# Performance work log

Measured on AMD Instinct MI355X. Metric: run time of the kernel, lower is better.

Reference implementation:

```python
import jax, jax.numpy as jnp
from jax import lax
import numpy as np

IMG = 800
SUB = 16
FS = IMG // SUB            # 50
NA = 9                     # 3 ratios x 3 scales
PRE_NMS = 6000             # test-mode n_test_pre_nms
POST_NMS = 300             # test-mode n_test_post_nms
NMS_THRESH = 0.7
MIN_BOX = 16.0
SLOPE = 0.01               # nn.LeakyReLU default


def build_anchors():
    # Faithful to _generate_anchor: x outer loop, y inner; ctr = grid - 8;
    # anchor rows are [x1, y1, w, h]; ratio outer, scale inner.
    c = np.arange(SUB, (FS + 1) * SUB, SUB).astype(np.float32) - 8.0  # 50 centers
    cx = np.repeat(c, FS)   # x is the outer loop
    cy = np.tile(c, FS)     # y is the inner loop
    rs = np.array([0.5, 1.0, 2.0], dtype=np.float32)
    ss = np.array([8.0, 16.0, 32.0], dtype=np.float32)
    hs = (SUB * ss[None, :] * np.sqrt(rs)[:, None]).reshape(-1)        # [9]
    ws = (SUB * ss[None, :] * np.sqrt(1.0 / rs)[:, None]).reshape(-1)  # [9]
    x1 = cx[:, None] - ws[None, :] / 2.0   # [2500, 9]
    y1 = cy[:, None] - hs[None, :] / 2.0
    w = np.broadcast_to(ws[None, :], x1.shape)
    h = np.broadcast_to(hs[None, :], x1.shape)
    return np.stack([x1, y1, w, h], axis=-1).reshape(-1, 4).astype(np.float32)  # [22500, 4]


def _conv(x, w, b, pad):
    y = lax.conv_general_dilated(x, w, (1, 1), ((pad, pad), (pad, pad)),
                                 dimension_numbers=("NCHW", "OIHW", "NCHW"))
    return y + b[None, :, None, None]


def _nms_keep(boxes):
    # Greedy NMS over score-sorted boxes [P,4] = (x1,y1,x2,y2); returns keep mask.
    x1, y1, x2, y2 = boxes[:, 0], boxes[:, 1], boxes[:, 2], boxes[:, 3]
    area = (x2 - x1 + 1.0) * (y2 - y1 + 1.0)
    P = boxes.shape[0]
    idx = jnp.arange(P)

    def body(i, keep):
        xx1 = jnp.maximum(x1[i], x1)
        yy1 = jnp.maximum(y1[i], y1)
        xx2 = jnp.minimum(x2[i], x2)
        yy2 = jnp.maximum(y2[i], y2)  # faithful to source bug: np.maximum, not minimum
        w = jnp.maximum(0.0, xx2 - xx1 + 1.0)
        h = jnp.maximum(0.0, yy2 - yy1 + 1.0)
        inter = w * h
        ov = inter / (area[i] + area - inter)
        suppress = (ov > NMS_THRESH) & (idx > i) & keep[i]
        return keep & ~suppress

    return lax.fori_loop(0, P, body, jnp.ones((P,), dtype=bool))


def _forward(in_features, conv_w, conv_b, reg_w, reg_b, cls_w, cls_b):
    B = in_features.shape[0]
    feat = _conv(in_features, conv_w, conv_b, 1)
    feat = jnp.where(feat >= 0, feat, SLOPE * feat)  # LeakyReLU(0.01)
    reg = _conv(feat, reg_w, reg_b, 0).transpose(0, 2, 3, 1).reshape(B, -1, 4)
    cls = _conv(feat, cls_w, cls_b, 0).transpose(0, 2, 3, 1).reshape(B, -1, 2)
    cls = jax.nn.softmax(cls, axis=2)

    anchors = jnp.asarray(build_anchors())  # [A,4] = (x1,y1,w,h)
    # The torch loop overwrites `rois` each batch iteration and returns only the
    # last batch's proposals; compute that directly.
    pr = reg[-1]                 # [A,4]
    score = cls[-1, :, 1]        # [A]
    hi = jnp.float32(IMG - 1)
    rx1 = jnp.clip(pr[:, 0] + anchors[:, 0], 0.0, hi)
    ry1 = jnp.clip(pr[:, 1] + anchors[:, 1], 0.0, hi)
    rx2 = jnp.clip(pr[:, 0] + anchors[:, 0] + pr[:, 2] + anchors[:, 2], 0.0, hi)
    ry2 = jnp.clip(pr[:, 1] + anchors[:, 1] + pr[:, 3] + anchors[:, 3], 0.0, hi)
    w = pr[:, 2] + anchors[:, 2]  # unclipped, as in source
    h = pr[:, 3] + anchors[:, 3]
    valid = (w >= MIN_BOX) & (h >= MIN_BOX)
    s = jnp.where(valid, score, -jnp.inf)   # filtered boxes sort to the end
    order = jnp.argsort(-s)[:PRE_NMS]       # top-6000 valid by objectness
    boxes = jnp.stack([rx1, ry1, rx2, ry2], axis=1)[order]  # [PRE,4]

    keep = _nms_keep(lax.stop_gradient(boxes))
    # first POST_NMS surviving boxes, in score order
    sel = jnp.argsort(jnp.where(keep, jnp.arange(PRE_NMS), PRE_NMS))[:POST_NMS]
    kb = boxes[sel]
    # output format: x1, y1, w, h
    return jnp.stack([kb[:, 0], kb[:, 1],
                      kb[:, 2] - kb[:, 0] + 1.0,
                      kb[:, 3] - kb[:, 1] + 1.0], axis=1)


def setup_inputs() -> dict:
    key = jax.random.key(0)
    k = jax.random.split(key, 4)
    return {
        "in_features": jax.random.normal(k[0], (8, 512, FS, FS), dtype=jnp.float32),
        "conv_w": jax.random.normal(k[1], (512, 512, 3, 3), dtype=jnp.float32) * 0.02,
        "conv_b": jnp.zeros((512,), dtype=jnp.float32),
        "reg_w": jax.random.normal(k[2], (36, 512, 1, 1), dtype=jnp.float32) * 0.02,
        "reg_b": jnp.zeros((36,), dtype=jnp.float32),
        "cls_w": jax.random.normal(k[3], (18, 512, 1, 1), dtype=jnp.float32) * 0.02,
        "cls_b": jnp.zeros((18,), dtype=jnp.float32),
    }


def reference(in_features, conv_w, conv_b, reg_w, reg_b, cls_w, cls_b):
    return _forward(in_features, conv_w, conv_b, reg_w, reg_b, cls_w, cls_b)
```

## Files before the change

### kernel.cpp

```cpp
#include <hip/hip_runtime.h>


#define NPIX 2500
#define NANCH 22500
#define NKEY 22528
#define PRE 6000
#define MASKW 94
#define MW 96
#define JCHUNK 1536
#define CS 8
#define KSLOT 8
#define PW 52
#define PSL 2704

__global__ __launch_bounds__(256) void prepK(
    const float* __restrict__ x,
    const float* __restrict__ wt,
    float* __restrict__ xpad,
    float* __restrict__ wtV)
{
    __shared__ float T[64][65];
    const int bx = blockIdx.x;
    if (bx < 512) {
        const int cin = bx;
        const float* src = x + (size_t)cin * NPIX;
        float* dst = xpad + (size_t)cin * PSL;
        for (int i = threadIdx.x; i < PSL; i += 256) {
            const int pr = i / PW;
            const int pc = i - pr * PW;
            float v = 0.f;
            if (pr >= 1 && pr <= 50 && pc >= 1 && pc <= 50)
                v = src[(pr - 1) * 50 + (pc - 1)];
            dst[i] = v;
        }
        return;
    }
    const int idx  = bx - 512;
    const int ct0  = (idx % 72) * 64;
    const int ocb  = (idx / 72) * 64;
    const int tid  = threadIdx.x;
    const int cidx = tid & 63;
    const int r4   = tid >> 6;
    #pragma unroll
    for (int i = 0; i < 16; ++i) {
        const int o = r4 + i * 4;
        T[o][cidx] = wt[(size_t)(ocb + o) * 4608 + ct0 + cidx];
    }
    __syncthreads();
    #pragma unroll
    for (int i = 0; i < 16; ++i) {
        const int ctl = ct0 + r4 + i * 4;
        const int cin = ctl / 9;
        const int t   = ctl - cin * 9;
        const int oc  = ocb + cidx;
        wtV[(((size_t)cin * 64 + (oc >> 3)) * 9 + t) * 8 + (oc & 7)] =
            T[cidx][r4 + i * 4];
    }
}

__global__ __launch_bounds__(256) void conv3x3_v9(
    const float* __restrict__ xpad,
    const float* __restrict__ wtV,
    float* __restrict__ part2)
{
    const int tid  = threadIdx.x;
    const int lane = tid & 63;
    const int wv   = tid >> 6;
    const int ocg  = blockIdx.x;
    const int pb   = blockIdx.y * 4 + wv;
    const int cing = blockIdx.z * 64;
    const int px0  = pb * 64 + lane;
    const int px1  = px0 + 1280;
    const bool act1 = (px1 < NPIX);
    const int r0 = px0 / 50, cc0 = px0 - r0 * 50;
    const int px1c = act1 ? px1 : 0;
    const int r1 = px1c / 50, cc1 = px1c - r1 * 50;

    const float* xb0 = xpad + (size_t)cing * PSL + (r0 + 1) * PW + (cc0 + 1);
    const float* xb1 = xpad + (size_t)cing * PSL + (r1 + 1) * PW + (cc1 + 1);

    float acc0[8], acc1[8];
    #pragma unroll
    for (int j = 0; j < 8; ++j) { acc0[j] = 0.f; acc1[j] = 0.f; }

    const float* wbase = wtV + ((size_t)cing * 64 + ocg) * 72;

    for (int cin = 0; cin < 64; ++cin) {
        float v0[9], v1[9];
        const float* xa = xb0 + (size_t)cin * PSL;
        const float* xc = xb1 + (size_t)cin * PSL;
        #pragma unroll
        for (int t = 0; t < 9; ++t) {
            const int dr = t / 3 - 1, dc = t % 3 - 1;
            v0[t] = xa[dr * PW + dc];
            v1[t] = xc[dr * PW + dc];
        }
        const float* wp = wbase + (size_t)cin * 4608;
        #pragma unroll
        for (int j = 0; j < 8; ++j) {
            float a = acc0[j];
            float b = acc1[j];
            #pragma unroll
            for (int t = 0; t < 9; ++t) {
                const float w = wp[t * 8 + j];
                a = fmaf(w, v0[t], a);
                b = fmaf(w, v1[t], b);
            }
            acc0[j] = a;
            acc1[j] = b;
        }
    }

    float* dst0 = part2 + ((size_t)blockIdx.z * 512 + ocg * 8) * NPIX + px0;
    #pragma unroll
    for (int j = 0; j < 8; ++j)
        dst0[(size_t)j * NPIX] = acc0[j];
    if (act1) {
        float* dst1 = part2 + ((size_t)blockIdx.z * 512 + ocg * 8) * NPIX + px1;
        #pragma unroll
        for (int j = 0; j < 8; ++j)
            dst1[(size_t)j * NPIX] = acc1[j];
    }
}

__global__ __launch_bounds__(256) void reduce_leaky4(
    const float* __restrict__ part2, const float* __restrict__ bias,
    float* __restrict__ feat)
{
    const int oc = blockIdx.x;
    const float b = bias[oc];
    float4* dstv = (float4*)(feat + (size_t)oc * NPIX);
    for (int q = threadIdx.x; q < 625; q += 256) {
        float4 s = make_float4(0.f, 0.f, 0.f, 0.f);
        #pragma unroll
        for (int k = 0; k < CS; ++k) {
            const float4 v = *(const float4*)(part2 + ((size_t)k * 512 + oc) * NPIX + q * 4);
            s.x += v.x; s.y += v.y; s.z += v.z; s.w += v.w;
        }
        s.x += b; s.y += b; s.z += b; s.w += b;
        s.x = (s.x >= 0.f) ? s.x : 0.01f * s.x;
        s.y = (s.y >= 0.f) ? s.y : 0.01f * s.y;
        s.z = (s.z >= 0.f) ? s.z : 0.01f * s.z;
        s.w = (s.w >= 0.f) ? s.w : 0.01f * s.w;
        dstv[q] = s;
    }
}

__global__ __launch_bounds__(256) void conv1x1_heads(
    const float* __restrict__ feat,
    const float* __restrict__ rw, const float* __restrict__ rb,
    const float* __restrict__ cw, const float* __restrict__ cb,
    float* __restrict__ regcls)
{
    __shared__ float sAcc[3][18][64];
    const int tid  = threadIdx.x;
    const int lane = tid & 63;
    const int wv   = tid >> 6;
    const int pix0 = blockIdx.x * 64 + lane;
    const bool act = (pix0 < NPIX);
    const int pix  = act ? pix0 : (NPIX - 1);
    const int chunk = blockIdx.y;
    const float* wb; const float* bb; int ocbase;
    if (chunk == 0)      { wb = rw;            bb = rb;      ocbase = 0;  }
    else if (chunk == 1) { wb = rw + 18 * 512; bb = rb + 18; ocbase = 18; }
    else                 { wb = cw;            bb = cb;      ocbase = 36; }

    float acc[18];
    #pragma unroll
    for (int k = 0; k < 18; ++k) acc[k] = 0.f;

    const int c0 = wv * 128;
    for (int cin = c0; cin < c0 + 128; ++cin) {
        const float v = feat[(size_t)cin * NPIX + pix];
        #pragma unroll
        for (int k = 0; k < 18; ++k)
            acc[k] = fmaf(wb[k * 512 + cin], v, acc[k]);
    }
    if (wv > 0) {
        #pragma unroll
        for (int k = 0; k < 18; ++k) sAcc[wv - 1][k][lane] = acc[k];
    }
    __syncthreads();
    if (wv == 0 && act) {
        #pragma unroll
        for (int k = 0; k < 18; ++k) {
            float s = acc[k];
            s += sAcc[0][k][lane];
            s += sAcc[1][k][lane];
            s += sAcc[2][k][lane];
            regcls[(size_t)(ocbase + k) * NPIX + pix] = s + bb[k];
        }
    }
}

__global__ __launch_bounds__(256) void decodeK(
    const float* __restrict__ regcls,
    float4* __restrict__ boxes,
    unsigned long long* __restrict__ keys)
{
    const int i = blockIdx.x * 256 + threadIdx.x;
    if (i >= NANCH) {
        if (i < NKEY) keys[i] = 0xFFFFFFFFFFFFFFFFull;
        return;
    }
    const int pos = i / 9;
    const int a   = i - pos * 9;
    const int hh  = pos / 50;
    const int wwp = pos - hh * 50;
    const int r = a / 3, s = a - r * 3;

    const float base_s[3] = {128.f, 256.f, 512.f};
    const float sq [3] = {0.70710678118654752440f, 1.0f, 1.41421356237309504880f};
    const float sqi[3] = {1.41421356237309504880f, 1.0f, 0.70710678118654752440f};
    const float hs = base_s[s] * sq[r];
    const float ws = base_s[s] * sqi[r];
    const float cx = (float)(hh * 16 + 8);
    const float cy = (float)(wwp * 16 + 8);
    const float ax = cx - ws * 0.5f;
    const float ay = cy - hs * 0.5f;

    const float pr0 = regcls[(size_t)(a * 4 + 0) * NPIX + pos];
    const float pr1 = regcls[(size_t)(a * 4 + 1) * NPIX + pos];
    const float pr2 = regcls[(size_t)(a * 4 + 2) * NPIX + pos];
    const float pr3 = regcls[(size_t)(a * 4 + 3) * NPIX + pos];
    const float c0  = regcls[(size_t)(36 + a * 2 + 0) * NPIX + pos];
    const float c1  = regcls[(size_t)(36 + a * 2 + 1) * NPIX + pos];

    const float m  = fmaxf(c0, c1);
    const float e0 = expf(c0 - m);
    const float e1 = expf(c1 - m);
    const float score = e1 / (e0 + e1);

    const float t0 = pr0 + ax;
    const float t1 = pr1 + ay;
    const float hi = 799.0f;
    const float rx1 = fminf(fmaxf(t0, 0.f), hi);
    const float ry1 = fminf(fmaxf(t1, 0.f), hi);
    const float rx2 = fminf(fmaxf((t0 + pr2) + ws, 0.f), hi);
    const float ry2 = fminf(fmaxf((t1 + pr3) + hs, 0.f), hi);
    const float bw = pr2 + ws;
    const float bh = pr3 + hs;
    const bool valid = (bw >= 16.f) && (bh >= 16.f);
    const float sc = valid ? score : -__builtin_inff();

    unsigned u = __float_as_uint(sc);
    u = (u & 0x80000000u) ? ~u : (u | 0x80000000u);
    const unsigned k32 = ~u;
    keys[i]  = ((unsigned long long)k32 << 32) | (unsigned)i;
    boxes[i] = make_float4(rx1, ry1, rx2, ry2);
}

__global__ __launch_bounds__(256) void rankK(
    const unsigned long long* __restrict__ keys, int* __restrict__ rank)
{
    const int i = blockIdx.x * 256 + threadIdx.x;
    const unsigned long long my = (i < NANCH) ? keys[i] : 0ull;
    const unsigned long long* kj = keys + blockIdx.y * 2816;
    int cnt = 0;
    for (int t = 0; t < 2816; t += 8) {
        #pragma unroll
        for (int q = 0; q < 8; ++q)
            cnt += (kj[t + q] < my) ? 1 : 0;
    }
    if (i < NANCH) atomicAdd(&rank[i], cnt);
}

__global__ __launch_bounds__(256) void scatterK(
    const float4* __restrict__ boxes, const int* __restrict__ rank,
    float4* __restrict__ sboxes)
{
    const int i = blockIdx.x * 256 + threadIdx.x;
    if (i < NANCH) {
        const int r = rank[i];
        if (r < PRE) sboxes[r] = boxes[i];
    }
}

__global__ __launch_bounds__(256) void nmsMaskK(
    const float4* __restrict__ sb, unsigned long long* __restrict__ mask)
{
    const int tid  = threadIdx.x;
    const int lane = tid & 63;
    const int wv   = tid >> 6;
    const int i0   = blockIdx.x * 16 + wv * 4;
    const int jbase = blockIdx.y * JCHUNK;

    float ix1[4], iy1[4], ix2[4], iy2[4], iar[4];
    #pragma unroll
    for (int ii = 0; ii < 4; ++ii) {
        const float4 b = sb[i0 + ii];
        ix1[ii] = b.x; iy1[ii] = b.y; ix2[ii] = b.z; iy2[ii] = b.w;
        iar[ii] = (b.z - b.x + 1.f) * (b.w - b.y + 1.f);
    }

    for (int w = 0; w < 24; ++w) {
        const int j  = jbase + w * 64 + lane;
        const int jc = (j < PRE) ? j : 0;
        const float4 bj = sb[jc];
        const float jar = (bj.z - bj.x + 1.f) * (bj.w - bj.y + 1.f);
        #pragma unroll
        for (int ii = 0; ii < 4; ++ii) {
            const int i = i0 + ii;
            const float xx1 = fmaxf(ix1[ii], bj.x);
            const float yy1 = fmaxf(iy1[ii], bj.y);
            const float xx2 = fminf(ix2[ii], bj.z);
            const float yy2 = fmaxf(iy2[ii], bj.w);
            const float wvv = fmaxf(0.f, xx2 - xx1 + 1.f);
            const float hvv = fmaxf(0.f, yy2 - yy1 + 1.f);
            const float inter = wvv * hvv;
            const float ov = inter / ((iar[ii] + jar) - inter);
            const bool pred = (j > i) && (j < PRE) && (ov > 0.7f);
            const unsigned long long bits = __ballot(pred);
            if (lane == 0)
                mask[(size_t)i * MW + blockIdx.y * 24 + w] = bits;
        }
    }
}

__global__ __launch_bounds__(64) void nmsScanOutK(
    const unsigned long long* __restrict__ mask,
    const float4* __restrict__ sb,
    float* __restrict__ out)
{
    __shared__ int sKept[300];
    __shared__ unsigned long long sKeepW[MASKW];
    const int lane = threadIdx.x;

    unsigned long long rem0 = 0ull, rem1 = 0ull;
    int cnt = 0;
    int done = 0;

    unsigned long long d00 = mask[(size_t)lane * MW + 0];
    unsigned long long d01 = mask[(size_t)lane * MW + 1];
    unsigned long long d11 = mask[(size_t)(64 + lane) * MW + 1];

    for (int p = 0; p < 47 && !done; ++p) {
        const int g0 = 2 * p, g1 = 2 * p + 1;

        unsigned long long n00 = 0ull, n01 = 0ull, n11 = 0ull;
        if (p + 1 < 47) {
            const int h0 = g0 + 2, h1 = g0 + 3;
            const int ra = h0 * 64 + lane;
            const int rb = h1 * 64 + lane;
            n00 = mask[(size_t)ra * MW + h0];
            n01 = mask[(size_t)ra * MW + h1];
            if (rb < PRE) n11 = mask[(size_t)rb * MW + h1];
        }

        unsigned long long cur0, cur1;
        {
            unsigned lo, hi;
            if (g0 < 64) {
                lo = __builtin_amdgcn_readlane((unsigned)rem0, g0);
                hi = __builtin_amdgcn_readlane((unsigned)(rem0 >> 32), g0);
            } else {
                lo = __builtin_amdgcn_readlane((unsigned)rem1, g0 - 64);
                hi = __builtin_amdgcn_readlane((unsigned)(rem1 >> 32), g0 - 64);
            }
            cur0 = ((unsigned long long)hi << 32) | lo;
            if (g1 < 64) {
                lo = __builtin_amdgcn_readlane((unsigned)rem0, g1);
                hi = __builtin_amdgcn_readlane((unsigned)(rem0 >> 32), g1);
            } else {
                lo = __builtin_amdgcn_readlane((unsigned)rem1, g1 - 64);
                hi = __builtin_amdgcn_readlane((unsigned)(rem1 >> 32), g1 - 64);
            }
            cur1 = ((unsigned long long)hi << 32) | lo;
        }
        const unsigned long long valid0 = ~0ull;
        const unsigned long long valid1 =
            (g1 == MASKW - 1) ? 0x0000FFFFFFFFFFFFull : ~0ull;

        unsigned long long kb0 = 0ull, kb1 = 0ull;
        for (;;) {
            const unsigned long long nd = (~cur0) & valid0;
            if (!nd) break;
            const int b = __builtin_ctzll(nd);
            if (lane == 0 && cnt < 300) sKept[cnt] = g0 * 64 + b;
            ++cnt;
            kb0 |= (1ull << b);
            if (cnt >= 300) { done = 1; break; }
            const unsigned al = __builtin_amdgcn_readlane((unsigned)d00, b);
            const unsigned ah = __builtin_amdgcn_readlane((unsigned)(d00 >> 32), b);
            const unsigned bl = __builtin_amdgcn_readlane((unsigned)d01, b);
            const unsigned bh = __builtin_amdgcn_readlane((unsigned)(d01 >> 32), b);
            cur0 |= (1ull << b) | (((unsigned long long)ah << 32) | al);
            cur1 |= (((unsigned long long)bh << 32) | bl);
        }
        if (!done) {
            for (;;) {
                const unsigned long long nd = (~cur1) & valid1;
                if (!nd) break;
                const int b = __builtin_ctzll(nd);
                if (lane == 0 && cnt < 300) sKept[cnt] = g1 * 64 + b;
                ++cnt;
                kb1 |= (1ull << b);
                if (cnt >= 300) { done = 1; break; }
                const unsigned cl = __builtin_amdgcn_readlane((unsigned)d11, b);
                const unsigned ch = __builtin_amdgcn_readlane((unsigned)(d11 >> 32), b);
                cur1 |= (1ull << b) | (((unsigned long long)ch << 32) | cl);
            }
        }
        if (lane == 0) { sKeepW[g0] = kb0; sKeepW[g1] = kb1; }

        if (!done && (kb0 | kb1)) {
            unsigned long long a0 = 0ull, a1 = 0ull;
            {
                int kbit[KSLOT];
                unsigned long long t = kb0;
                #pragma unroll
                for (int s = 0; s < KSLOT; ++s) {
                    kbit[s] = t ? __builtin_ctzll(t) : 64;
                    t &= t - 1;
                }
                #pragma unroll
                for (int s = 0; s < KSLOT; ++s) {
                    if (kbit[s] < 64) {
                        const unsigned long long* pr =
                            mask + (size_t)(g0 * 64 + kbit[s]) * MW;
                        a0 |= pr[lane];
                        a1 |= (lane < MASKW - 64) ? pr[64 + lane] : 0ull;
                    }
                }
                while (t) {
                    const int b = __builtin_ctzll(t); t &= t - 1;
                    const unsigned long long* pr =
                        mask + (size_t)(g0 * 64 + b) * MW;
                    a0 |= pr[lane];
                    a1 |= (lane < MASKW - 64) ? pr[64 + lane] : 0ull;
                }
            }
            {
                int kbit[KSLOT];
                unsigned long long t = kb1;
                #pragma unroll
                for (int s = 0; s < KSLOT; ++s) {
                    kbit[s] = t ? __builtin_ctzll(t) : 64;
                    t &= t - 1;
                }
                #pragma unroll
                for (int s = 0; s < KSLOT; ++s) {
                    if (kbit[s] < 64) {
                        const unsigned long long* pr =
                            mask + (size_t)(g1 * 64 + kbit[s]) * MW;
                        a0 |= pr[lane];
                        a1 |= (lane < MASKW - 64) ? pr[64 + lane] : 0ull;
                    }
                }
                while (t) {
                    const int b = __builtin_ctzll(t); t &= t - 1;
                    const unsigned long long* pr =
                        mask + (size_t)(g1 * 64 + b) * MW;
                    a0 |= pr[lane];
                    a1 |= (lane < MASKW - 64) ? pr[64 + lane] : 0ull;
                }
            }
            rem0 |= a0;
            rem1 |= a1;
        }
        d00 = n00; d01 = n01; d11 = n11;
    }

    __syncthreads();

    if (cnt < 300) {
        int c = cnt;
        for (int g = 0; g < MASKW && c < 300; ++g) {
            const unsigned long long valid =
                (g == MASKW - 1) ? 0x0000FFFFFFFFFFFFull : ~0ull;
            unsigned long long u = (~sKeepW[g]) & valid;
            while (u && c < 300) {
                const int b = __builtin_ctzll(u); u &= u - 1;
                if (lane == 0) sKept[c] = g * 64 + b;
                ++c;
            }
        }
    }
    __syncthreads();

    for (int s = lane; s < 300; s += 64) {
        const float4 b = sb[sKept[s]];
        out[s * 4 + 0] = b.x;
        out[s * 4 + 1] = b.y;
        out[s * 4 + 2] = b.z - b.x + 1.0f;
        out[s * 4 + 3] = b.w - b.y + 1.0f;
    }
}

extern "C" void kernel_launch(void* const* d_in, const int* in_sizes, int n_in,
                              void* d_out, int out_size, void* d_ws, size_t ws_size,
                              hipStream_t stream)
{
    (void)in_sizes; (void)n_in; (void)out_size; (void)ws_size;
    const float* x   = (const float*)d_in[0] + (size_t)7 * 512 * NPIX;
    const float* cw3 = (const float*)d_in[1];
    const float* cb3 = (const float*)d_in[2];
    const float* rw  = (const float*)d_in[3];
    const float* rb  = (const float*)d_in[4];
    const float* clw = (const float*)d_in[5];
    const float* clb = (const float*)d_in[6];
    float* out = (float*)d_out;

    char* p = (char*)d_ws;
    auto alloc = [&](size_t n) { char* r = p; p += (n + 255) & ~(size_t)255; return r; };
    float*  part2  = (float*)alloc((size_t)CS * 512 * NPIX * 4);
    float*  wtV    = (float*)alloc((size_t)4608 * 512 * 4);
    float*  xpad   = (float*)alloc((size_t)512 * PSL * 4);
    float*  feat   = (float*)alloc((size_t)512 * NPIX * 4);
    float*  regcls = (float*)alloc((size_t)54 * NPIX * 4);
    float4* boxes  = (float4*)alloc((size_t)NANCH * 16);
    unsigned long long* keys = (unsigned long long*)alloc((size_t)NKEY * 8);
    int*    rank   = (int*)alloc((size_t)NANCH * 4);
    float4* sboxes = (float4*)alloc((size_t)PRE * 16);
    unsigned long long* mask = (unsigned long long*)alloc((size_t)PRE * MW * 8);

    hipMemsetAsync(rank, 0, (size_t)NANCH * 4, stream);
    prepK         <<<1088, 256, 0, stream>>>(x, cw3, xpad, wtV);
    conv3x3_v9    <<<dim3(64, 5, CS), 256, 0, stream>>>(xpad, wtV, part2);
    reduce_leaky4 <<<512, 256, 0, stream>>>(part2, cb3, feat);
    conv1x1_heads <<<dim3(40, 3), 256, 0, stream>>>(feat, rw, rb, clw, clb, regcls);
    decodeK       <<<88, 256, 0, stream>>>(regcls, boxes, keys);
    rankK         <<<dim3(88, 8), 256, 0, stream>>>(keys, rank);
    scatterK      <<<88, 256, 0, stream>>>(boxes, rank, sboxes);
    nmsMaskK      <<<dim3(375, 4), 256, 0, stream>>>(sboxes, mask);
    nmsScanOutK   <<<1, 64, 0, stream>>>(mask, sboxes, out);
}
```

Measured before the change: 501.7 us.

## Double-buffer conv input loads, split head conv over more blocks, fold rank memset

The 3x3 conv loop now prefetches the next input channel's 3x3 patch into a second register set while the current channel's FMAs run. This hides global load latency at the cost of more registers. The 1x1 head conv splits its 18 output channels across three z-blocks, so it launches 360 blocks instead of 120 for better occupancy. The hipMemsetAsync of the rank buffer is removed, and decodeK zeroes rank instead, saving one launch.

New measurement: 468.8 us. 6.6% less time.

```diff
diff --git a/kernel.cpp b/kernel.cpp
--- a/kernel.cpp
+++ b/kernel.cpp
@@ -58,7 +58,7 @@
     }
 }
 
-__global__ __launch_bounds__(256) void conv3x3_v9(
+__global__ __launch_bounds__(256) void conv3x3_v11(
     const float* __restrict__ xpad,
     const float* __restrict__ wtV,
     float* __restrict__ part2)
@@ -85,29 +85,66 @@
 
     const float* wbase = wtV + ((size_t)cing * 64 + ocg) * 72;
 
-    for (int cin = 0; cin < 64; ++cin) {
-        float v0[9], v1[9];
-        const float* xa = xb0 + (size_t)cin * PSL;
-        const float* xc = xb1 + (size_t)cin * PSL;
-        #pragma unroll
-        for (int t = 0; t < 9; ++t) {
-            const int dr = t / 3 - 1, dc = t % 3 - 1;
-            v0[t] = xa[dr * PW + dc];
-            v1[t] = xc[dr * PW + dc];
-        }
-        const float* wp = wbase + (size_t)cin * 4608;
-        #pragma unroll
-        for (int j = 0; j < 8; ++j) {
-            float a = acc0[j];
-            float b = acc1[j];
+    float vA0[9], vA1[9], vB0[9], vB1[9];
+    #pragma unroll
+    for (int t = 0; t < 9; ++t) {
+        const int dr = t / 3 - 1, dc = t % 3 - 1;
+        vA0[t] = xb0[dr * PW + dc];
+        vA1[t] = xb1[dr * PW + dc];
+    }
+
+    for (int cin = 0; cin < 64; cin += 2) {
+        {
+            const float* xa = xb0 + (size_t)(cin + 1) * PSL;
+            const float* xc = xb1 + (size_t)(cin + 1) * PSL;
             #pragma unroll
             for (int t = 0; t < 9; ++t) {
-                const float w = wp[t * 8 + j];
-                a = fmaf(w, v0[t], a);
-                b = fmaf(w, v1[t], b);
-            }
-            acc0[j] = a;
-            acc1[j] = b;
+                const int dr = t / 3 - 1, dc = t % 3 - 1;
+                vB0[t] = xa[dr * PW + dc];
+                vB1[t] = xc[dr * PW + dc];
+            }
+        }
+        {
+            const float* wp = wbase + (size_t)cin * 4608;
+            #pragma unroll
+            for (int j = 0; j < 8; ++j) {
+                float a = acc0[j];
+                float b = acc1[j];
+                #pragma unroll
+                for (int t = 0; t < 9; ++t) {
+                    const float w = wp[t * 8 + j];
+                    a = fmaf(w, vA0[t], a);
+                    b = fmaf(w, vA1[t], b);
+                }
+                acc0[j] = a;
+                acc1[j] = b;
+            }
+        }
+        if (cin + 2 < 64) {
+            const float* xa = xb0 + (size_t)(cin + 2) * PSL;
+            const float* xc = xb1 + (size_t)(cin + 2) * PSL;
+            #pragma unroll
+            for (int t = 0; t < 9; ++t) {
+                const int dr = t / 3 - 1, dc = t % 3 - 1;
+                vA0[t] = xa[dr * PW + dc];
+                vA1[t] = xc[dr * PW + dc];
+            }
+        }
+        {
+            const float* wp = wbase + (size_t)(cin + 1) * 4608;
+            #pragma unroll
+            for (int j = 0; j < 8; ++j) {
+                float a = acc0[j];
+                float b = acc1[j];
+                #pragma unroll
+                for (int t = 0; t < 9; ++t) {
+                    const float w = wp[t * 8 + j];
+                    a = fmaf(w, vB0[t], a);
+                    b = fmaf(w, vB1[t], b);
+                }
+                acc0[j] = a;
+                acc1[j] = b;
+            }
         }
     }
 
@@ -152,7 +189,7 @@
     const float* __restrict__ cw, const float* __restrict__ cb,
     float* __restrict__ regcls)
 {
-    __shared__ float sAcc[3][18][64];
+    __shared__ float sAcc[3][6][64];
     const int tid  = threadIdx.x;
     const int lane = tid & 63;
     const int wv   = tid >> 6;
@@ -160,35 +197,36 @@
     const bool act = (pix0 < NPIX);
     const int pix  = act ? pix0 : (NPIX - 1);
     const int chunk = blockIdx.y;
+    const int k0    = blockIdx.z * 6;
     const float* wb; const float* bb; int ocbase;
     if (chunk == 0)      { wb = rw;            bb = rb;      ocbase = 0;  }
     else if (chunk == 1) { wb = rw + 18 * 512; bb = rb + 18; ocbase = 18; }
     else                 { wb = cw;            bb = cb;      ocbase = 36; }
 
-    float acc[18];
-    #pragma unroll
-    for (int k = 0; k < 18; ++k) acc[k] = 0.f;
+    float acc[6];
+    #pragma unroll
+    for (int k = 0; k < 6; ++k) acc[k] = 0.f;
 
     const int c0 = wv * 128;
     for (int cin = c0; cin < c0 + 128; ++cin) {
         const float v = feat[(size_t)cin * NPIX + pix];
         #pragma unroll
-        for (int k = 0; k < 18; ++k)
-            acc[k] = fmaf(wb[k * 512 + cin], v, acc[k]);
+        for (int k = 0; k < 6; ++k)
+            acc[k] = fmaf(wb[(k0 + k) * 512 + cin], v, acc[k]);
     }
     if (wv > 0) {
         #pragma unroll
-        for (int k = 0; k < 18; ++k) sAcc[wv - 1][k][lane] = acc[k];
+        for (int k = 0; k < 6; ++k) sAcc[wv - 1][k][lane] = acc[k];
     }
     __syncthreads();
     if (wv == 0 && act) {
         #pragma unroll
-        for (int k = 0; k < 18; ++k) {
+        for (int k = 0; k < 6; ++k) {
             float s = acc[k];
             s += sAcc[0][k][lane];
             s += sAcc[1][k][lane];
             s += sAcc[2][k][lane];
-            regcls[(size_t)(ocbase + k) * NPIX + pix] = s + bb[k];
+            regcls[(size_t)(ocbase + k0 + k) * NPIX + pix] = s + bb[k0 + k];
         }
     }
 }
@@ -196,9 +234,11 @@
 __global__ __launch_bounds__(256) void decodeK(
     const float* __restrict__ regcls,
     float4* __restrict__ boxes,
-    unsigned long long* __restrict__ keys)
+    unsigned long long* __restrict__ keys,
+    int* __restrict__ rank)
 {
     const int i = blockIdx.x * 256 + threadIdx.x;
+    if (i < NANCH) rank[i] = 0;
     if (i >= NANCH) {
         if (i < NKEY) keys[i] = 0xFFFFFFFFFFFFFFFFull;
         return;
@@ -514,12 +554,11 @@
     float4* sboxes = (float4*)alloc((size_t)PRE * 16);
     unsigned long long* mask = (unsigned long long*)alloc((size_t)PRE * MW * 8);
 
-    hipMemsetAsync(rank, 0, (size_t)NANCH * 4, stream);
     prepK         <<<1088, 256, 0, stream>>>(x, cw3, xpad, wtV);
-    conv3x3_v9    <<<dim3(64, 5, CS), 256, 0, stream>>>(xpad, wtV, part2);
+    conv3x3_v11   <<<dim3(64, 5, CS), 256, 0, stream>>>(xpad, wtV, part2);
     reduce_leaky4 <<<512, 256, 0, stream>>>(part2, cb3, feat);
-    conv1x1_heads <<<dim3(40, 3), 256, 0, stream>>>(feat, rw, rb, clw, clb, regcls);
-    decodeK       <<<88, 256, 0, stream>>>(regcls, boxes, keys);
+    conv1x1_heads <<<dim3(40, 3, 3), 256, 0, stream>>>(feat, rw, rb, clw, clb, regcls);
+    decodeK       <<<88, 256, 0, stream>>>(regcls, boxes, keys, rank);
     rankK         <<<dim3(88, 8), 256, 0, stream>>>(keys, rank);
     scatterK      <<<88, 256, 0, stream>>>(boxes, rank, sboxes);
     nmsMaskK      <<<dim3(375, 4), 256, 0, stream>>>(sboxes, mask);
```

## Compute two adjacent pixels per thread in conv3x3, split 1x1 heads, fold rank memset

Applied to the files above, without the earlier changes.

The 3x3 conv now gives each thread two horizontally adjacent output pixels instead of two pixels 1280 apart. The overlapping input window can then be read as six float2 loads rather than eighteen scalar loads, and the outputs are stored as float2. The 1x1 head kernel gains a z-dimension that splits the 18 output channels into three groups of six, which triples the grid and cuts per-thread register work. The rank memset is folded into decodeK to remove one API call.

Result: no change. 505.0 us (+0.7%).

```diff
diff --git a/kernel.cpp b/kernel.cpp
--- a/kernel.cpp
+++ b/kernel.cpp
@@ -58,7 +58,7 @@
     }
 }
 
-__global__ __launch_bounds__(256) void conv3x3_v9(
+__global__ __launch_bounds__(256) void conv3x3_v12(
     const float* __restrict__ xpad,
     const float* __restrict__ wtV,
     float* __restrict__ part2)
@@ -69,15 +69,13 @@
     const int ocg  = blockIdx.x;
     const int pb   = blockIdx.y * 4 + wv;
     const int cing = blockIdx.z * 64;
-    const int px0  = pb * 64 + lane;
-    const int px1  = px0 + 1280;
-    const bool act1 = (px1 < NPIX);
-    const int r0 = px0 / 50, cc0 = px0 - r0 * 50;
-    const int px1c = act1 ? px1 : 0;
-    const int r1 = px1c / 50, cc1 = px1c - r1 * 50;
-
-    const float* xb0 = xpad + (size_t)cing * PSL + (r0 + 1) * PW + (cc0 + 1);
-    const float* xb1 = xpad + (size_t)cing * PSL + (r1 + 1) * PW + (cc1 + 1);
+    const int pq   = pb * 64 + lane;
+    const bool act = (pq < 1250);
+    const int pqc  = act ? pq : 0;
+    const int r    = pqc / 25;
+    const int c    = (pqc - r * 25) * 2;
+
+    const float* xb = xpad + (size_t)cing * PSL + r * PW + c;
 
     float acc0[8], acc1[8];
     #pragma unroll
@@ -86,40 +84,36 @@
     const float* wbase = wtV + ((size_t)cing * 64 + ocg) * 72;
 
     for (int cin = 0; cin < 64; ++cin) {
-        float v0[9], v1[9];
-        const float* xa = xb0 + (size_t)cin * PSL;
-        const float* xc = xb1 + (size_t)cin * PSL;
-        #pragma unroll
-        for (int t = 0; t < 9; ++t) {
-            const int dr = t / 3 - 1, dc = t % 3 - 1;
-            v0[t] = xa[dr * PW + dc];
-            v1[t] = xc[dr * PW + dc];
-        }
+        const float* xr = xb + (size_t)cin * PSL;
+        const float2 w00 = *(const float2*)(xr);
+        const float2 w01 = *(const float2*)(xr + 2);
+        const float2 w10 = *(const float2*)(xr + PW);
+        const float2 w11 = *(const float2*)(xr + PW + 2);
+        const float2 w20 = *(const float2*)(xr + 2 * PW);
+        const float2 w21 = *(const float2*)(xr + 2 * PW + 2);
+
         const float* wp = wbase + (size_t)cin * 4608;
         #pragma unroll
         for (int j = 0; j < 8; ++j) {
-            float a = acc0[j];
-            float b = acc1[j];
-            #pragma unroll
-            for (int t = 0; t < 9; ++t) {
-                const float w = wp[t * 8 + j];
-                a = fmaf(w, v0[t], a);
-                b = fmaf(w, v1[t], b);
-            }
-            acc0[j] = a;
-            acc1[j] = b;
-        }
-    }
-
-    float* dst0 = part2 + ((size_t)blockIdx.z * 512 + ocg * 8) * NPIX + px0;
-    #pragma unroll
-    for (int j = 0; j < 8; ++j)
-        dst0[(size_t)j * NPIX] = acc0[j];
-    if (act1) {
-        float* dst1 = part2 + ((size_t)blockIdx.z * 512 + ocg * 8) * NPIX + px1;
+            float a = acc0[j], b = acc1[j];
+            const float t0 = wp[0 * 8 + j]; a = fmaf(t0, w00.x, a); b = fmaf(t0, w00.y, b);
+            const float t1 = wp[1 * 8 + j]; a = fmaf(t1, w00.y, a); b = fmaf(t1, w01.x, b);
+            const float t2 = wp[2 * 8 + j]; a = fmaf(t2, w01.x, a); b = fmaf(t2, w01.y, b);
+            const float t3 = wp[3 * 8 + j]; a = fmaf(t3, w10.x, a); b = fmaf(t3, w10.y, b);
+            const float t4 = wp[4 * 8 + j]; a = fmaf(t4, w10.y, a); b = fmaf(t4, w11.x, b);
+            const float t5 = wp[5 * 8 + j]; a = fmaf(t5, w11.x, a); b = fmaf(t5, w11.y, b);
+            const float t6 = wp[6 * 8 + j]; a = fmaf(t6, w20.x, a); b = fmaf(t6, w20.y, b);
+            const float t7 = wp[7 * 8 + j]; a = fmaf(t7, w20.y, a); b = fmaf(t7, w21.x, b);
+            const float t8 = wp[8 * 8 + j]; a = fmaf(t8, w21.x, a); b = fmaf(t8, w21.y, b);
+            acc0[j] = a; acc1[j] = b;
+        }
+    }
+
+    if (act) {
+        float* dst = part2 + ((size_t)blockIdx.z * 512 + ocg * 8) * NPIX + 2 * pq;
         #pragma unroll
         for (int j = 0; j < 8; ++j)
-            dst1[(size_t)j * NPIX] = acc1[j];
+            *(float2*)(dst + (size_t)j * NPIX) = make_float2(acc0[j], acc1[j]);
     }
 }
 
@@ -152,7 +146,7 @@
     const float* __restrict__ cw, const float* __restrict__ cb,
     float* __restrict__ regcls)
 {
-    __shared__ float sAcc[3][18][64];
+    __shared__ float sAcc[3][6][64];
     const int tid  = threadIdx.x;
     const int lane = tid & 63;
     const int wv   = tid >> 6;
@@ -160,35 +154,36 @@
     const bool act = (pix0 < NPIX);
     const int pix  = act ? pix0 : (NPIX - 1);
     const int chunk = blockIdx.y;
+    const int k0    = blockIdx.z * 6;
     const float* wb; const float* bb; int ocbase;
     if (chunk == 0)      { wb = rw;            bb = rb;      ocbase = 0;  }
     else if (chunk == 1) { wb = rw + 18 * 512; bb = rb + 18; ocbase = 18; }
     else                 { wb = cw;            bb = cb;      ocbase = 36; }
 
-    float acc[18];
+    float acc[6];
     #pragma unroll
-    for (int k = 0; k < 18; ++k) acc[k] = 0.f;
+    for (int k = 0; k < 6; ++k) acc[k] = 0.f;
 
     const int c0 = wv * 128;
     for (int cin = c0; cin < c0 + 128; ++cin) {
         const float v = feat[(size_t)cin * NPIX + pix];
         #pragma unroll
-        for (int k = 0; k < 18; ++k)
-            acc[k] = fmaf(wb[k * 512 + cin], v, acc[k]);
+        for (int k = 0; k < 6; ++k)
+            acc[k] = fmaf(wb[(k0 + k) * 512 + cin], v, acc[k]);
     }
     if (wv > 0) {
         #pragma unroll
-        for (int k = 0; k < 18; ++k) sAcc[wv - 1][k][lane] = acc[k];
+        for (int k = 0; k < 6; ++k) sAcc[wv - 1][k][lane] = acc[k];
     }
     __syncthreads();
     if (wv == 0 && act) {
         #pragma unroll
-        for (int k = 0; k < 18; ++k) {
+        for (int k = 0; k < 6; ++k) {
             float s = acc[k];
             s += sAcc[0][k][lane];
             s += sAcc[1][k][lane];
             s += sAcc[2][k][lane];
-            regcls[(size_t)(ocbase + k) * NPIX + pix] = s + bb[k];
+            regcls[(size_t)(ocbase + k0 + k) * NPIX + pix] = s + bb[k0 + k];
         }
     }
 }
@@ -196,9 +191,11 @@
 __global__ __launch_bounds__(256) void decodeK(
     const float* __restrict__ regcls,
     float4* __restrict__ boxes,
-    unsigned long long* __restrict__ keys)
+    unsigned long long* __restrict__ keys,
+    int* __restrict__ rank)
 {
     const int i = blockIdx.x * 256 + threadIdx.x;
+    if (i < NANCH) rank[i] = 0;
     if (i >= NANCH) {
         if (i < NKEY) keys[i] = 0xFFFFFFFFFFFFFFFFull;
         return;
@@ -514,12 +511,11 @@
     float4* sboxes = (float4*)alloc((size_t)PRE * 16);
     unsigned long long* mask = (unsigned long long*)alloc((size_t)PRE * MW * 8);
 
-    hipMemsetAsync(rank, 0, (size_t)NANCH * 4, stream);
     prepK         <<<1088, 256, 0, stream>>>(x, cw3, xpad, wtV);
-    conv3x3_v9    <<<dim3(64, 5, CS), 256, 0, stream>>>(xpad, wtV, part2);
+    conv3x3_v12   <<<dim3(64, 5, CS), 256, 0, stream>>>(xpad, wtV, part2);
     reduce_leaky4 <<<512, 256, 0, stream>>>(part2, cb3, feat);
-    conv1x1_heads <<<dim3(40, 3), 256, 0, stream>>>(feat, rw, rb, clw, clb, regcls);
-    decodeK       <<<88, 256, 0, stream>>>(regcls, boxes, keys);
+    conv1x1_heads <<<dim3(40, 3, 3), 256, 0, stream>>>(feat, rw, rb, clw, clb, regcls);
+    decodeK       <<<88, 256, 0, stream>>>(regcls, boxes, keys, rank);
     rankK         <<<dim3(88, 8), 256, 0, stream>>>(keys, rank);
     scatterK      <<<88, 256, 0, stream>>>(boxes, rank, sboxes);
     nmsMaskK      <<<dim3(375, 4), 256, 0, stream>>>(sboxes, mask);
```
